# Performance work log

Measured on AMD Instinct MI355X. Metric: run time of the kernel, lower is better.

The kernel has to match this reference:

```python
import jax, jax.numpy as jnp
from jax import lax
import numpy as np

WS = 32          # window size
NUM_AA = 21      # one-hot alphabet size (hardcoded in original forward)
L = 2048         # sequence length
WIDTH = 2048
IN_SIZE = WS * NUM_AA + WS  # 704


def setup_inputs() -> dict:
    key = jax.random.key(0)
    ks = jax.random.split(key, 8)
    x = jax.random.randint(ks[0], (L,), 0, NUM_AA, dtype=jnp.int32)
    gain = np.sqrt(2.0)  # relu gain, xavier_normal init
    def xavier(k, fan_out, fan_in):
        std = gain * np.sqrt(2.0 / (fan_in + fan_out))
        return jax.random.normal(k, (fan_out, fan_in), dtype=jnp.float32) * std
    inp = {"x": x}
    dims = [(WIDTH, IN_SIZE), (WIDTH, WIDTH), (WIDTH, WIDTH), (WIDTH, WIDTH), (WIDTH, WIDTH), (1, WIDTH)]
    for i, (fo, fi) in enumerate(dims):
        inp[f"W{i}"] = xavier(ks[i + 1], fo, fi)
        inp[f"b{i}"] = jnp.zeros((fo,), dtype=jnp.float32)
    return inp


def reference(x, W0, b0, W1, b1, W2, b2, W3, b3, W4, b4, W5, b5):
    Ws = (W0, W1, W2, W3, W4, W5)
    bs = (b0, b1, b2, b3, b4, b5)
    n = x.shape[0]
    # one-hot features; the sliding window of the last WS one-hots is
    onehot = jax.nn.one_hot(x, NUM_AA, dtype=jnp.float32)          # [n, 21]
    padded = jnp.concatenate([jnp.zeros((WS - 1, NUM_AA), jnp.float32), onehot], axis=0)
    idx = jnp.arange(n)[:, None] + jnp.arange(WS)[None, :]          # [n, WS]
    xfeat = padded[idx].reshape(n, WS * NUM_AA)                     # [n, 672]

    def step(y_window, xf):
        # y_window: last WS predictions (init zeros, matching original)
        h = jnp.concatenate([xf, y_window])                         # [704]
        for W, b in zip(Ws, bs):
            h = jax.nn.relu(W @ h + b)  # relu after EVERY layer incl. output
        y_window = jnp.concatenate([y_window[1:], h])               # h: [1]
        return y_window, h[0]

    _, ys = lax.scan(step, jnp.zeros((WS,), jnp.float32), xfeat)
    return ys  # [n] predictions, equivalent of torch.cat(y_pred[ws:])
```

## Files before the change

kernel.cpp:

```cpp
#include <hip/hip_runtime.h>
#include <stdint.h>


typedef uint32_t u32;
typedef unsigned long long ull;
typedef _Float16 half_t;
typedef _Float16 half2_t __attribute__((ext_vector_type(2)));

#define L_SEQ 2048
#define WIDTH 2048
#define WS    32
#define NAA   21
#define INS   704
#define NB    256
#define SLP_FAIL 2
#define SLP_IDLE 16
#define N_IDLE_H 8
#define N_IDLE_0 6

__device__ __forceinline__ float h2f(u32 b){
  union { unsigned short u; half_t h; } c; c.u = (unsigned short)(b & 0xffffu);
  return (float)c.h;
}
__device__ __forceinline__ u32 f2h(float f){
  union { unsigned short u; half_t h; } c; c.h = (half_t)f;
  return (u32)c.u;
}
__device__ __forceinline__ float fdot2f(u32 a, u32 b, float c){
#if __has_builtin(__builtin_amdgcn_fdot2)
  union { u32 u; half2_t v; } ca, cb; ca.u = a; cb.u = b;
  return __builtin_amdgcn_fdot2(ca.v, cb.v, c, false);
#else
  return c + h2f(a)*h2f(b) + h2f(a>>16)*h2f(b>>16);
#endif
}
__device__ __forceinline__ u32 aload(const u32* p){
  return __hip_atomic_load(const_cast<u32*>(p), __ATOMIC_RELAXED, __HIP_MEMORY_SCOPE_AGENT);
}
__device__ __forceinline__ void astore(u32* p, u32 v){
  __hip_atomic_store(p, v, __ATOMIC_RELAXED, __HIP_MEMORY_SCOPE_AGENT);
}
__device__ __forceinline__ ull aload64(const ull* p){
  return __hip_atomic_load(const_cast<ull*>(p), __ATOMIC_RELAXED, __HIP_MEMORY_SCOPE_AGENT);
}
__device__ __forceinline__ void astore64(ull* p, ull v){
  __hip_atomic_store(p, v, __ATOMIC_RELAXED, __HIP_MEMORY_SCOPE_AGENT);
}

__device__ __forceinline__ void load8(const u32* base, u32 (&r)[8]){
  #pragma unroll
  for (int k=0;k<8;++k) r[k] = aload(base + 256*k);
}
__device__ __forceinline__ bool chk8(const u32 (&r)[8], u32 tag){
  bool ok = true;
  #pragma unroll
  for (int k=0;k<8;++k) ok &= ((r[k] >> 16) == tag);
  return ok;
}
__device__ __forceinline__ void pollb(const u32* base, u32 tag, u32 (&rec)[8]){
  for(;;){
    load8(base, rec);
    if (chk8(rec, tag)) return;
    __builtin_amdgcn_s_sleep(SLP_FAIL);
  }
}
__device__ __forceinline__ ull poll1q(const ull* p, u32 tag){
  for(;;){
    ull a = aload64(p);
    if ((u32)(a >> 32) == tag) return a;
  }
}

__global__ void k_wt(const float* __restrict__ W0, float* __restrict__ W0T){
  int tid = blockIdx.x*256 + threadIdx.x;
  if (tid < INS*WIDTH){
    int c = tid >> 11, i = tid & 2047;
    W0T[(size_t)c*WIDTH + i] = W0[(size_t)i*INS + c];
  }
}

__global__ void k_wc(const float* __restrict__ A, const float* __restrict__ B,
                     const float* __restrict__ C, const float* __restrict__ D,
                     uint4* __restrict__ Wp){
  int b = blockIdx.x; int l = b >> 11; int r = b & 2047; int j = threadIdx.x;
  const float* S = (l==0)?A:(l==1)?B:(l==2)?C:D;
  const float* row = S + (size_t)r*WIDTH;
  u32 o[4];
  #pragma unroll
  for (int q=0;q<4;++q)
    o[q] = f2h(row[256*(2*q)+j]) | (f2h(row[256*(2*q+1)+j]) << 16);
  Wp[(size_t)b*256 + j] = make_uint4(o[0],o[1],o[2],o[3]);
}

__global__ void k_c0(const int* __restrict__ x, const float* __restrict__ W0T,
                     const float* __restrict__ b0, uint4* __restrict__ c0p){
  int t = blockIdx.x, j = threadIdx.x;
  __shared__ int cidx[WS];
  if (j < WS){
    int s = t - (WS-1) + j;
    cidx[j] = (s >= 0) ? (NAA*j + x[s]) : -1;
  }
  __syncthreads();
  float acc[8];
  #pragma unroll
  for (int k=0;k<8;++k) acc[k] = b0[256*k + j];
  for (int m=0;m<WS;++m){
    int c = cidx[m];
    if (c >= 0){
      const float* col = W0T + (size_t)c*WIDTH;
      #pragma unroll
      for (int k=0;k<8;++k) acc[k] += col[256*k + j];
    }
  }
  u32 o[4];
  #pragma unroll
  for (int q=0;q<4;++q) o[q] = f2h(acc[2*q]) | (f2h(acc[2*q+1]) << 16);
  c0p[(size_t)t*256 + j] = make_uint4(o[0],o[1],o[2],o[3]);
}

__global__ void k_wy(const float* __restrict__ W0, u32* __restrict__ wyb){
  int b = blockIdx.x; int k = b >> 4, p = b & 15; int j = threadIdx.x;
  int col = 256*k + j;
  float a = W0[(size_t)col*INS + (INS-WS) + 2*p];
  float c = W0[(size_t)col*INS + (INS-WS) + 2*p + 1];
  wyb[(size_t)b*256 + j] = f2h(a) | (f2h(c) << 16);
}

__global__ void k_reset(u32* __restrict__ hb, u32* __restrict__ pq){
  int tid = blockIdx.x*256 + threadIdx.x;
  if (tid < 3*WIDTH) hb[tid] = 0xFFFFFFFFu;
  if (tid < 128)     pq[tid] = 0xFFFFFFFFu;
}

__global__ __launch_bounds__(256, 1) void k_main(
    const float* __restrict__ W0,
    const float* __restrict__ b1, const float* __restrict__ b2,
    const float* __restrict__ b3, const float* __restrict__ b4,
    const float* __restrict__ W5, const float* __restrict__ b5p,
    const uint4* __restrict__ Wp, const uint4* __restrict__ c0p,
    const u32* __restrict__ wyb,
    u32* hb, ull* pbq, float* __restrict__ out)
{
  const int j  = threadIdx.x;
  const int X  = blockIdx.x;
  const int g  = X >> 6;
  const int Xl = X & 63;
  const int lw = j & 63;
  const int w  = j >> 6;

  __shared__ float red[2][4][32];

  uint4 wreg[32];
  #pragma unroll
  for (int r=0;r<32;++r)
    wreg[r] = Wp[((size_t)g*2048 + 32*Xl + r)*256 + j];

  const float* bp = (g==0)?b1:(g==1)?b2:(g==2)?b3:b4;
  float bv = 0.f;
  if (j < 32) bv = bp[32*Xl + j];
  float w5v = 0.f;
  if (g == 3 && j < 32) w5v = W5[32*Xl + j];

  u32 hh[4];

  auto dotsbfly = [&](int buf){
    float c32[32];
    #pragma unroll
    for (int r=0;r<32;++r){
      float a = 0.f;
      a = fdot2f(wreg[r].x, hh[0], a);
      a = fdot2f(wreg[r].y, hh[1], a);
      a = fdot2f(wreg[r].z, hh[2], a);
      a = fdot2f(wreg[r].w, hh[3], a);
      c32[r] = a;
    }
    float c16[16];
    #pragma unroll
    for (int i=0;i<16;++i){
      float v = c32[2*i]   + __shfl_xor(c32[2*i],   1);
      float u = c32[2*i+1] + __shfl_xor(c32[2*i+1], 1);
      c16[i] = (lw & 1) ? u : v;
    }
    float c8[8];
    #pragma unroll
    for (int i=0;i<8;++i){
      float v = c16[2*i]   + __shfl_xor(c16[2*i],   2);
      float u = c16[2*i+1] + __shfl_xor(c16[2*i+1], 2);
      c8[i] = (lw & 2) ? u : v;
    }
    float c4[4];
    #pragma unroll
    for (int i=0;i<4;++i){
      float v = c8[2*i]   + __shfl_xor(c8[2*i],   4);
      float u = c8[2*i+1] + __shfl_xor(c8[2*i+1], 4);
      c4[i] = (lw & 4) ? u : v;
    }
    float c2[2];
    #pragma unroll
    for (int i=0;i<2;++i){
      float v = c4[2*i]   + __shfl_xor(c4[2*i],   8);
      float u = c4[2*i+1] + __shfl_xor(c4[2*i+1], 8);
      c2[i] = (lw & 8) ? u : v;
    }
    float v1 = c2[0] + __shfl_xor(c2[0], 16);
    float u1 = c2[1] + __shfl_xor(c2[1], 16);
    float c1 = (lw & 16) ? u1 : v1;
    float tot = c1 + __shfl_xor(c1, 32);
    if (lw < 32) red[buf][w][lw] = tot;
  };

  for (int i=0;i<g;++i) __builtin_amdgcn_s_sleep(SLP_IDLE);

  if (g == 3){
    const u32* base = hb + (size_t)2*WIDTH + j;
    u32 rec[8];
    #pragma unroll 1
    for (int t=0; t<L_SEQ; ++t){
      const int buf = t & 1;
      pollb(base, (u32)t, rec);
      #pragma unroll
      for (int q=0;q<4;++q) hh[q] = (rec[2*q] & 0xffffu) | (rec[2*q+1] << 16);
      dotsbfly(buf);
      __syncthreads();
      if (j < 32){
        float s = fmaxf(red[buf][0][j]+red[buf][1][j]+red[buf][2][j]+red[buf][3][j] + bv, 0.f);
        float pp = s * w5v;
        pp += __shfl_xor(pp, 1);
        pp += __shfl_xor(pp, 2);
        pp += __shfl_xor(pp, 4);
        pp += __shfl_xor(pp, 8);
        pp += __shfl_xor(pp, 16);
        if (j == 0)
          astore64(pbq + Xl, ((ull)(u32)t << 32) | (ull)__float_as_uint(pp));
      }
      for (int i=0;i<N_IDLE_H;++i) __builtin_amdgcn_s_sleep(SLP_IDLE);
    }
  } else if (g > 0){
    const u32* base = hb + (size_t)(g-1)*WIDTH + j;
    u32 rec[8];
    #pragma unroll 1
    for (int t=0; t<L_SEQ; ++t){
      const int buf = t & 1;
      pollb(base, (u32)t, rec);
      #pragma unroll
      for (int q=0;q<4;++q) hh[q] = (rec[2*q] & 0xffffu) | (rec[2*q+1] << 16);
      dotsbfly(buf);
      __syncthreads();
      if (j < 32){
        float s = fmaxf(red[buf][0][j]+red[buf][1][j]+red[buf][2][j]+red[buf][3][j] + bv, 0.f);
        astore(&hb[(size_t)g*WIDTH + 32*Xl + j], ((u32)t << 16) | f2h(s));
      }
      for (int i=0;i<N_IDLE_H;++i) __builtin_amdgcn_s_sleep(SLP_IDLE);
    }
  } else {
    float w31v[8];
    #pragma unroll
    for (int k=0;k<8;++k)
      w31v[k] = W0[(size_t)(256*k + j)*INS + (INS-1)];
    const float b5v = b5p[0];
    u32 yqp[16];
    #pragma unroll
    for (int p=0;p<16;++p) yqp[p] = 0u;
    float u_part[8];
    #pragma unroll
    for (int k=0;k<8;++k) u_part[k] = 0.f;
    const ull* ybase = pbq + lw;

    #pragma unroll 1
    for (int t=0; t<L_SEQ; ++t){
      const int buf = t & 1;
      uint4 c0v = c0p[(size_t)t*256 + j];
      float y = 0.f;
      if (t > 0){
        ull pv = poll1q(ybase, (u32)(t-1));
        float p = __uint_as_float((u32)pv);
        #pragma unroll
        for (int d=1; d<64; d<<=1) p += __shfl_xor(p, d);
        y = fmaxf(p + b5v, 0.f);
        if (X == 0 && j == 0) out[t-1] = y;
        yqp[15] |= (f2h(y) << 16);
      }
      {
        u32 c0h[4] = { c0v.x, c0v.y, c0v.z, c0v.w };
        float h0v[8];
        #pragma unroll
        for (int q=0;q<4;++q){
          h0v[2*q]   = fmaxf(h2f(c0h[q])       + u_part[2*q]   + w31v[2*q]*y,   0.f);
          h0v[2*q+1] = fmaxf(h2f(c0h[q] >> 16) + u_part[2*q+1] + w31v[2*q+1]*y, 0.f);
        }
        #pragma unroll
        for (int q=0;q<4;++q) hh[q] = f2h(h0v[2*q]) | (f2h(h0v[2*q+1]) << 16);
      }
      dotsbfly(buf);
      __syncthreads();
      if (j < 32){
        float s = fmaxf(red[buf][0][j]+red[buf][1][j]+red[buf][2][j]+red[buf][3][j] + bv, 0.f);
        astore(&hb[32*Xl + j], ((u32)t << 16) | f2h(s));
      }
      {
        #pragma unroll
        for (int p=0;p<15;++p) yqp[p] = (yqp[p] >> 16) | (yqp[p+1] << 16);
        yqp[15] = (yqp[15] >> 16);
        #pragma unroll
        for (int k=0;k<8;++k){
          float a = 0.f;
          #pragma unroll
          for (int p=0;p<16;++p)
            a = fdot2f(wyb[(size_t)(16*k+p)*256 + j], yqp[p], a);
          u_part[k] = a;
        }
      }
      for (int i=0;i<N_IDLE_0;++i) __builtin_amdgcn_s_sleep(SLP_IDLE);
    }

    if (X == 0){
      ull pv = poll1q(ybase, (u32)(L_SEQ-1));
      float p = __uint_as_float((u32)pv);
      #pragma unroll
      for (int d=1; d<64; d<<=1) p += __shfl_xor(p, d);
      if (j == 0) out[L_SEQ-1] = fmaxf(p + b5v, 0.f);
    }
  }
}

extern "C" void kernel_launch(void* const* d_in, const int* in_sizes, int n_in,
                              void* d_out, int out_size, void* d_ws, size_t ws_size,
                              hipStream_t stream) {
  (void)in_sizes; (void)n_in; (void)out_size; (void)ws_size;
  const int*   x  = (const int*)  d_in[0];
  const float* W0 = (const float*)d_in[1];
  const float* b0 = (const float*)d_in[2];
  const float* W1 = (const float*)d_in[3];
  const float* b1 = (const float*)d_in[4];
  const float* W2 = (const float*)d_in[5];
  const float* b2 = (const float*)d_in[6];
  const float* W3 = (const float*)d_in[7];
  const float* b3 = (const float*)d_in[8];
  const float* W4 = (const float*)d_in[9];
  const float* b4 = (const float*)d_in[10];
  const float* W5 = (const float*)d_in[11];
  const float* b5 = (const float*)d_in[12];
  float* out = (float*)d_out;
  char*  ws  = (char*)d_ws;

  constexpr size_t OFF_WP  = 0;
  constexpr size_t OFF_C0  = 33554432;
  constexpr size_t OFF_W0T = 41943040;
  constexpr size_t OFF_WY  = 47710208;
  constexpr size_t OFF_HB  = 47841280;
  constexpr size_t OFF_PQ  = 47865856;

  uint4* Wp  = (uint4*)(ws + OFF_WP);
  uint4* c0p = (uint4*)(ws + OFF_C0);
  float* W0T = (float*)(ws + OFF_W0T);
  u32*   wyb = (u32*)  (ws + OFF_WY);
  u32*   hb  = (u32*)  (ws + OFF_HB);
  u32*   pq  = (u32*)  (ws + OFF_PQ);
  ull*   pbq = (ull*)  (ws + OFF_PQ);

  k_wt   <<<5632, 256, 0, stream>>>(W0, W0T);
  k_wc   <<<8192, 256, 0, stream>>>(W1, W2, W3, W4, Wp);
  k_c0   <<<2048, 256, 0, stream>>>(x, W0T, b0, c0p);
  k_wy   <<<128,  256, 0, stream>>>(W0, wyb);
  k_reset<<<32,   256, 0, stream>>>(hb, pq);
  k_main <<<NB,   256, 0, stream>>>(W0, b1, b2, b3, b4, W5, b5,
                                    Wp, c0p, wyb, hb, pbq, out);
}
```

Baseline: 22.98 ms.

## Replicate inter-block activation buffers to spread polling contention across addresses

Each layer's fp16 activation vector is now written into 16 replicated copies (and the final-layer partials into 64 replicas), so groups of 4 consumer blocks poll their own copy instead of all 64 blocks hammering one buffer. All 256 threads now take part in the write-out, with the bias kept in LDS. The sleep between failed polls is removed and the idle sleeps are retuned. The cost is extra store traffic per step and tighter spin loops that may add memory pressure.

Measured after the change: 19.66 ms, median of 2. -14.4%, faster.

```diff
diff --git a/kernel.cpp b/kernel.cpp
--- a/kernel.cpp
+++ b/kernel.cpp
@@ -13,10 +13,9 @@
 #define NAA   21
 #define INS   704
 #define NB    256
-#define SLP_FAIL 2
-#define SLP_IDLE 16
-#define N_IDLE_H 8
-#define N_IDLE_0 6
+#define NREP  16
+#define SLP_IDLE 20
+#define N_IDLE   3
 
 __device__ __forceinline__ float h2f(u32 b){
   union { unsigned short u; half_t h; } c; c.u = (unsigned short)(b & 0xffffu);
@@ -45,30 +44,6 @@
 }
 __device__ __forceinline__ void astore64(ull* p, ull v){
   __hip_atomic_store(p, v, __ATOMIC_RELAXED, __HIP_MEMORY_SCOPE_AGENT);
-}
-
-__device__ __forceinline__ void load8(const u32* base, u32 (&r)[8]){
-  #pragma unroll
-  for (int k=0;k<8;++k) r[k] = aload(base + 256*k);
-}
-__device__ __forceinline__ bool chk8(const u32 (&r)[8], u32 tag){
-  bool ok = true;
-  #pragma unroll
-  for (int k=0;k<8;++k) ok &= ((r[k] >> 16) == tag);
-  return ok;
-}
-__device__ __forceinline__ void pollb(const u32* base, u32 tag, u32 (&rec)[8]){
-  for(;;){
-    load8(base, rec);
-    if (chk8(rec, tag)) return;
-    __builtin_amdgcn_s_sleep(SLP_FAIL);
-  }
-}
-__device__ __forceinline__ ull poll1q(const ull* p, u32 tag){
-  for(;;){
-    ull a = aload64(p);
-    if ((u32)(a >> 32) == tag) return a;
-  }
 }
 
 __global__ void k_wt(const float* __restrict__ W0, float* __restrict__ W0T){
@@ -126,10 +101,10 @@
   wyb[(size_t)b*256 + j] = f2h(a) | (f2h(c) << 16);
 }
 
-__global__ void k_reset(u32* __restrict__ hb, u32* __restrict__ pq){
+__global__ void k_reset(u32* __restrict__ hr, u32* __restrict__ pr){
   int tid = blockIdx.x*256 + threadIdx.x;
-  if (tid < 3*WIDTH) hb[tid] = 0xFFFFFFFFu;
-  if (tid < 128)     pq[tid] = 0xFFFFFFFFu;
+  if (tid < 3*NREP*2048) hr[tid] = 0xFFFFFFFFu;
+  if (tid < 8192)        pr[tid] = 0xFFFFFFFFu;
 }
 
 __global__ __launch_bounds__(256, 1) void k_main(
@@ -139,7 +114,7 @@
     const float* __restrict__ W5, const float* __restrict__ b5p,
     const uint4* __restrict__ Wp, const uint4* __restrict__ c0p,
     const u32* __restrict__ wyb,
-    u32* hb, ull* pbq, float* __restrict__ out)
+    u32* hrep, ull* prep, float* __restrict__ out)
 {
   const int j  = threadIdx.x;
   const int X  = blockIdx.x;
@@ -147,32 +122,33 @@
   const int Xl = X & 63;
   const int lw = j & 63;
   const int w  = j >> 6;
+  const int r  = j & 31;
 
   __shared__ float red[2][4][32];
+  __shared__ float bias_lds[32];
 
   uint4 wreg[32];
   #pragma unroll
-  for (int r=0;r<32;++r)
-    wreg[r] = Wp[((size_t)g*2048 + 32*Xl + r)*256 + j];
+  for (int i=0;i<32;++i)
+    wreg[i] = Wp[((size_t)g*2048 + 32*Xl + i)*256 + j];
 
   const float* bp = (g==0)?b1:(g==1)?b2:(g==2)?b3:b4;
-  float bv = 0.f;
-  if (j < 32) bv = bp[32*Xl + j];
-  float w5v = 0.f;
-  if (g == 3 && j < 32) w5v = W5[32*Xl + j];
+  if (j < 32) bias_lds[j] = bp[32*Xl + j];
+  float w5r = 0.f;
+  if (g == 3) w5r = W5[32*Xl + r];
 
   u32 hh[4];
 
   auto dotsbfly = [&](int buf){
     float c32[32];
     #pragma unroll
-    for (int r=0;r<32;++r){
+    for (int i=0;i<32;++i){
       float a = 0.f;
-      a = fdot2f(wreg[r].x, hh[0], a);
-      a = fdot2f(wreg[r].y, hh[1], a);
-      a = fdot2f(wreg[r].z, hh[2], a);
-      a = fdot2f(wreg[r].w, hh[3], a);
-      c32[r] = a;
+      a = fdot2f(wreg[i].x, hh[0], a);
+      a = fdot2f(wreg[i].y, hh[1], a);
+      a = fdot2f(wreg[i].z, hh[2], a);
+      a = fdot2f(wreg[i].w, hh[3], a);
+      c32[i] = a;
     }
     float c16[16];
     #pragma unroll
@@ -209,48 +185,61 @@
     if (lw < 32) red[buf][w][lw] = tot;
   };
 
+  auto pollrec = [&](const u32* base, u32 tag, u32 (&rec)[8]){
+    for(;;){
+      #pragma unroll
+      for (int k=0;k<8;++k) rec[k] = aload(base + 256*k);
+      bool ok = true;
+      #pragma unroll
+      for (int k=0;k<8;++k) ok &= ((rec[k] >> 16) == tag);
+      if (ok) break;
+    }
+  };
+
   for (int i=0;i<g;++i) __builtin_amdgcn_s_sleep(SLP_IDLE);
 
   if (g == 3){
-    const u32* base = hb + (size_t)2*WIDTH + j;
-    u32 rec[8];
+    const u32* base = hrep + ((size_t)2*NREP + (Xl>>2))*2048 + j;
     #pragma unroll 1
     for (int t=0; t<L_SEQ; ++t){
       const int buf = t & 1;
-      pollb(base, (u32)t, rec);
+      u32 rec[8];
+      pollrec(base, (u32)t, rec);
       #pragma unroll
       for (int q=0;q<4;++q) hh[q] = (rec[2*q] & 0xffffu) | (rec[2*q+1] << 16);
       dotsbfly(buf);
       __syncthreads();
-      if (j < 32){
-        float s = fmaxf(red[buf][0][j]+red[buf][1][j]+red[buf][2][j]+red[buf][3][j] + bv, 0.f);
-        float pp = s * w5v;
-        pp += __shfl_xor(pp, 1);
-        pp += __shfl_xor(pp, 2);
-        pp += __shfl_xor(pp, 4);
-        pp += __shfl_xor(pp, 8);
-        pp += __shfl_xor(pp, 16);
-        if (j == 0)
-          astore64(pbq + Xl, ((ull)(u32)t << 32) | (ull)__float_as_uint(pp));
-      }
-      for (int i=0;i<N_IDLE_H;++i) __builtin_amdgcn_s_sleep(SLP_IDLE);
+      float s = fmaxf(red[buf][0][r]+red[buf][1][r]+red[buf][2][r]+red[buf][3][r]
+                      + bias_lds[r], 0.f);
+      float pp = s * w5r;
+      pp += __shfl_xor(pp, 1);
+      pp += __shfl_xor(pp, 2);
+      pp += __shfl_xor(pp, 4);
+      pp += __shfl_xor(pp, 8);
+      pp += __shfl_xor(pp, 16);
+      if (w == 0)
+        astore64(prep + (size_t)lw*64 + Xl,
+                 ((ull)(u32)t << 32) | (ull)__float_as_uint(pp));
+      for (int i=0;i<N_IDLE;++i) __builtin_amdgcn_s_sleep(SLP_IDLE);
     }
   } else if (g > 0){
-    const u32* base = hb + (size_t)(g-1)*WIDTH + j;
-    u32 rec[8];
+    const u32* base = hrep + ((size_t)(g-1)*NREP + (Xl>>2))*2048 + j;
+    u32* dst = hrep + (size_t)g*NREP*2048;
     #pragma unroll 1
     for (int t=0; t<L_SEQ; ++t){
       const int buf = t & 1;
-      pollb(base, (u32)t, rec);
+      u32 rec[8];
+      pollrec(base, (u32)t, rec);
       #pragma unroll
       for (int q=0;q<4;++q) hh[q] = (rec[2*q] & 0xffffu) | (rec[2*q+1] << 16);
       dotsbfly(buf);
       __syncthreads();
-      if (j < 32){
-        float s = fmaxf(red[buf][0][j]+red[buf][1][j]+red[buf][2][j]+red[buf][3][j] + bv, 0.f);
-        astore(&hb[(size_t)g*WIDTH + 32*Xl + j], ((u32)t << 16) | f2h(s));
-      }
-      for (int i=0;i<N_IDLE_H;++i) __builtin_amdgcn_s_sleep(SLP_IDLE);
+      float s = fmaxf(red[buf][0][r]+red[buf][1][r]+red[buf][2][r]+red[buf][3][r]
+                      + bias_lds[r], 0.f);
+      u32 rv = ((u32)t << 16) | f2h(s);
+      astore(dst + (size_t)((j>>5)    )*2048 + 32*Xl + r, rv);
+      astore(dst + (size_t)((j>>5) + 8)*2048 + 32*Xl + r, rv);
+      for (int i=0;i<N_IDLE;++i) __builtin_amdgcn_s_sleep(SLP_IDLE);
     }
   } else {
     float w31v[8];
@@ -264,7 +253,8 @@
     float u_part[8];
     #pragma unroll
     for (int k=0;k<8;++k) u_part[k] = 0.f;
-    const ull* ybase = pbq + lw;
+    const ull* yb = prep + (size_t)Xl*64 + lw;
+    u32* dst = hrep;
 
     #pragma unroll 1
     for (int t=0; t<L_SEQ; ++t){
@@ -272,8 +262,10 @@
       uint4 c0v = c0p[(size_t)t*256 + j];
       float y = 0.f;
       if (t > 0){
-        ull pv = poll1q(ybase, (u32)(t-1));
-        float p = __uint_as_float((u32)pv);
+        const u32 tag = (u32)(t-1);
+        ull v;
+        for(;;){ v = aload64(yb); if ((u32)(v >> 32) == tag) break; }
+        float p = __uint_as_float((u32)v);
         #pragma unroll
         for (int d=1; d<64; d<<=1) p += __shfl_xor(p, d);
         y = fmaxf(p + b5v, 0.f);
@@ -293,10 +285,11 @@
       }
       dotsbfly(buf);
       __syncthreads();
-      if (j < 32){
-        float s = fmaxf(red[buf][0][j]+red[buf][1][j]+red[buf][2][j]+red[buf][3][j] + bv, 0.f);
-        astore(&hb[32*Xl + j], ((u32)t << 16) | f2h(s));
-      }
+      float s = fmaxf(red[buf][0][r]+red[buf][1][r]+red[buf][2][r]+red[buf][3][r]
+                      + bias_lds[r], 0.f);
+      u32 rv = ((u32)t << 16) | f2h(s);
+      astore(dst + (size_t)((j>>5)    )*2048 + 32*Xl + r, rv);
+      astore(dst + (size_t)((j>>5) + 8)*2048 + 32*Xl + r, rv);
       {
         #pragma unroll
         for (int p=0;p<15;++p) yqp[p] = (yqp[p] >> 16) | (yqp[p+1] << 16);
@@ -310,12 +303,14 @@
           u_part[k] = a;
         }
       }
-      for (int i=0;i<N_IDLE_0;++i) __builtin_amdgcn_s_sleep(SLP_IDLE);
-    }
-
-    if (X == 0){
-      ull pv = poll1q(ybase, (u32)(L_SEQ-1));
-      float p = __uint_as_float((u32)pv);
+      for (int i=0;i<N_IDLE;++i) __builtin_amdgcn_s_sleep(SLP_IDLE);
+    }
+
+    if (X == 0 && j < 64){
+      const u32 tag = (u32)(L_SEQ-1);
+      ull v;
+      for(;;){ v = aload64(yb); if ((u32)(v >> 32) == tag) break; }
+      float p = __uint_as_float((u32)v);
       #pragma unroll
       for (int d=1; d<64; d<<=1) p += __shfl_xor(p, d);
       if (j == 0) out[L_SEQ-1] = fmaxf(p + b5v, 0.f);
@@ -346,23 +341,23 @@
   constexpr size_t OFF_WP  = 0;
   constexpr size_t OFF_C0  = 33554432;
   constexpr size_t OFF_W0T = 41943040;
+  constexpr size_t OFF_HR  = 41943040;
+  constexpr size_t OFF_PR  = 42336256;
   constexpr size_t OFF_WY  = 47710208;
-  constexpr size_t OFF_HB  = 47841280;
-  constexpr size_t OFF_PQ  = 47865856;
 
   uint4* Wp  = (uint4*)(ws + OFF_WP);
   uint4* c0p = (uint4*)(ws + OFF_C0);
   float* W0T = (float*)(ws + OFF_W0T);
+  u32*   hr  = (u32*)  (ws + OFF_HR);
+  u32*   pr  = (u32*)  (ws + OFF_PR);
+  ull*   prq = (ull*)  (ws + OFF_PR);
   u32*   wyb = (u32*)  (ws + OFF_WY);
-  u32*   hb  = (u32*)  (ws + OFF_HB);
-  u32*   pq  = (u32*)  (ws + OFF_PQ);
-  ull*   pbq = (ull*)  (ws + OFF_PQ);
 
   k_wt   <<<5632, 256, 0, stream>>>(W0, W0T);
   k_wc   <<<8192, 256, 0, stream>>>(W1, W2, W3, W4, Wp);
   k_c0   <<<2048, 256, 0, stream>>>(x, W0T, b0, c0p);
   k_wy   <<<128,  256, 0, stream>>>(W0, wyb);
-  k_reset<<<32,   256, 0, stream>>>(hb, pq);
+  k_reset<<<384,  256, 0, stream>>>(hr, pr);
   k_main <<<NB,   256, 0, stream>>>(W0, b1, b2, b3, b4, W5, b5,
-                                    Wp, c0p, wyb, hb, pbq, out);
-}
+                                    Wp, c0p, wyb, hr, prq, out);
+}
```
